# Kernel tuning notes

Measured on AMD Instinct MI355X. Metric: run time of the kernel, lower is better.

The kernel has to match this reference:

```python
import jax, jax.numpy as jnp
import numpy as np

N, H, E = 16384, 1024, 8


def setup_inputs() -> dict:
    key = jax.random.key(0)
    ks = jax.random.split(key, 6)
    scale = 0.02
    tokens = jax.random.normal(ks[0], (N, H), dtype=jnp.float32)
    gate_w = jax.random.normal(ks[1], (E, H), dtype=jnp.float32) * scale  # torch Linear weight [out,in]
    w1 = jax.random.normal(ks[2], (E, H, H), dtype=jnp.float32) * scale   # per-expert first Linear [out,in]
    b1 = jax.random.normal(ks[3], (E, H), dtype=jnp.float32) * scale
    w2 = jax.random.normal(ks[4], (E, H, H), dtype=jnp.float32) * scale   # per-expert second Linear [out,in]
    b2 = jax.random.normal(ks[5], (E, H), dtype=jnp.float32) * scale
    return {"tokens": tokens, "gate_w": gate_w, "w1": w1, "b1": b1, "w2": w2, "b2": b2}


def reference(tokens, gate_w, w1, b1, w2, b2):
    # gate: logits [N,E], top-1 routing (output is NOT scaled by gate weight, matching the torch module)
    logits = jnp.einsum('nh,eh->ne', tokens, gate_w)
    weights = jax.nn.softmax(logits, axis=-1)
    top1 = jnp.argmax(weights, axis=-1)                     # [N] int
    onehot = jax.nn.one_hot(top1, w1.shape[0], dtype=tokens.dtype)  # [N,E]
    out = jnp.zeros_like(tokens)
    for e in range(w1.shape[0]):  # small fixed expert count
        h = jax.nn.relu(jnp.einsum('nh,fh->nf', tokens, w1[e]) + b1[e])
        y = jnp.einsum('nf,gf->ng', h, w2[e]) + b2[e]
        out = out + onehot[:, e:e + 1] * y
    return out
```

## Files before the change

### kernel.cpp

```cpp
#include <hip/hip_runtime.h>
#include <hip/hip_bf16.h>
#include <stdint.h>

#define N_TOK 16384
#define HDIM  1024
#define NE    8

#define BM 128
#define BN 128
#define BK 64
#define NKT (HDIM / BK)
#define NT_N (HDIM / BN)
#define MAXTILES (N_TOK / BM + NE)
#define GRID_GEMM (MAXTILES * NT_N)

typedef __attribute__((ext_vector_type(8))) short          bf16x8;
typedef __attribute__((ext_vector_type(8))) unsigned short ushort8;
typedef __attribute__((ext_vector_type(4))) unsigned short ushort4v;
typedef __attribute__((ext_vector_type(4))) float          f32x4;

__device__ __forceinline__ unsigned short f2bf(float f) {
  union { float f; uint32_t u; } c; c.f = f;
  uint32_t u = c.u;
  uint32_t r = (u + 0x7fffu + ((u >> 16) & 1u)) >> 16;
  return (unsigned short)r;
}

__device__ __forceinline__ void gload_lds16(const void* g, void* l) {
  __builtin_amdgcn_global_load_lds((const __attribute__((address_space(1))) void*)g,
                                   (__attribute__((address_space(3))) void*)l, 16, 0, 0);
}

__device__ __forceinline__ void expert_range(const int* __restrict__ counts, int e,
                                             int& base, int& cnt) {
  int run = 0; base = 0; cnt = 0;
#pragma unroll
  for (int i = 0; i < NE; ++i) {
    int c = counts[i];
    if (i == e) { base = run; cnt = c; }
    run += c;
  }
}

__global__ __launch_bounds__(256) void gate_kernel(
    const float* __restrict__ tokens, const float* __restrict__ gate_w,
    unsigned short* __restrict__ tokB, int* __restrict__ eid)
{
  int wid  = threadIdx.x >> 6;
  int lane = threadIdx.x & 63;
  int n    = blockIdx.x * 4 + wid;

  const float* trow = tokens + (size_t)n * HDIM;
  float4 x[4];
#pragma unroll
  for (int i = 0; i < 4; ++i)
    x[i] = *(const float4*)(trow + i * 256 + lane * 4);

  unsigned short* drow = tokB + (size_t)n * HDIM;
#pragma unroll
  for (int i = 0; i < 4; ++i) {
    ushort4v o;
    o[0] = f2bf(x[i].x); o[1] = f2bf(x[i].y);
    o[2] = f2bf(x[i].z); o[3] = f2bf(x[i].w);
    *(ushort4v*)(drow + i * 256 + lane * 4) = o;
  }

  double acc[NE];
#pragma unroll
  for (int e = 0; e < NE; ++e) {
    const float* grow = gate_w + e * HDIM;
    double a = 0.0;
#pragma unroll
    for (int i = 0; i < 4; ++i) {
      float4 g = *(const float4*)(grow + i * 256 + lane * 4);
      a += (double)x[i].x * g.x + (double)x[i].y * g.y
         + (double)x[i].z * g.z + (double)x[i].w * g.w;
    }
    acc[e] = a;
  }
#pragma unroll
  for (int off = 32; off; off >>= 1) {
#pragma unroll
    for (int e = 0; e < NE; ++e) acc[e] += __shfl_xor(acc[e], off);
  }
  if (lane == 0) {
    int best = 0; double bv = acc[0];
#pragma unroll
    for (int e = 1; e < NE; ++e) if (acc[e] > bv) { bv = acc[e]; best = e; }
    eid[n] = best;
  }
}

__global__ __launch_bounds__(256) void rank_kernel(
    const int* __restrict__ eid, int* __restrict__ rank, int* __restrict__ counts)
{
  __shared__ int h[NE];
  __shared__ int bbase[NE];
  int t = threadIdx.x;
  int n = blockIdx.x * 256 + t;
  if (t < NE) h[t] = 0;
  __syncthreads();
  int e = eid[n];
  int r = atomicAdd(&h[e], 1);
  __syncthreads();
  if (t < NE) bbase[t] = atomicAdd(&counts[t], h[t]);
  __syncthreads();
  rank[n] = bbase[e] + r;
}

__global__ __launch_bounds__(256) void perm_kernel(
    const int* __restrict__ counts, const int* __restrict__ eid,
    const int* __restrict__ rank, int* __restrict__ topos)
{
  __shared__ int off[NE];
  int t = threadIdx.x;
  if (t == 0) {
    int run = 0;
#pragma unroll
    for (int e = 0; e < NE; ++e) { off[e] = run; run += counts[e]; }
  }
  __syncthreads();
  int n = blockIdx.x * 256 + t;
  topos[off[eid[n]] + rank[n]] = n;
}

__global__ void tilemap_kernel(const int* __restrict__ counts, int* __restrict__ tmeta) {
  if (threadIdx.x == 0) {
    int idx = 0;
    for (int e = 0; e < NE; ++e) {
      int ntile = (counts[e] + BM - 1) / BM;
      for (int mt = 0; mt < ntile; ++mt) tmeta[1 + idx++] = (mt << 3) | e;
    }
    tmeta[0] = idx;
  }
}

__global__ __launch_bounds__(256) void cvt2_kernel(
    const float* __restrict__ w1, const float* __restrict__ w2,
    unsigned short* __restrict__ w1B, unsigned short* __restrict__ w2B)
{
  int b = blockIdx.x;
  const float* src; unsigned short* dst; size_t i;
  if (b < 4096) { src = w1; dst = w1B; i = (size_t)b * 256 + threadIdx.x; }
  else          { src = w2; dst = w2B; i = (size_t)(b - 4096) * 256 + threadIdx.x; }
  const float4* s = (const float4*)src + i * 2;
  float4 a = s[0], c = s[1];
  ushort8 o;
  o[0] = f2bf(a.x); o[1] = f2bf(a.y); o[2] = f2bf(a.z); o[3] = f2bf(a.w);
  o[4] = f2bf(c.x); o[5] = f2bf(c.y); o[6] = f2bf(c.z); o[7] = f2bf(c.w);
  ((ushort8*)dst)[i] = o;
}

#define GEMM_PREAMBLE()                                                        \
  int bid = blockIdx.x;                                                        \
  int logical = (bid & 7) * (GRID_GEMM / 8) + (bid >> 3);                      \
  int tile = logical >> 3;                                                     \
  int nt   = logical & 7;                                                      \
  if (tile >= tmeta[0]) return;                                                \
  int ent = tmeta[1 + tile];                                                   \
  int e = ent & 7, mt = ent >> 3;                                              \
  int base, cnt;                                                               \
  expert_range(counts, e, base, cnt);                                          \
  __shared__ unsigned short Alds[BM * BK];                                     \
  __shared__ unsigned short Blds[BN * BK];                                     \
  int t    = threadIdx.x;                                                      \
  int kc   = t & 7;                                  \
  int rowi = t >> 3;                                                \
  int sch  = kc ^ (rowi & 7);               \
  int lane = t & 63, wid = t >> 6;                                             \
  int wr = wid >> 1, wc = wid & 1;                                             \
  f32x4 acc[4][4] = {};                                                        \
  int arow0 = wr * 64 + (lane & 15);                                           \
  int brow0 = wc * 64 + (lane & 15);                                           \
  int hi    = lane >> 4;                                             \
  int xo    = lane & 7;

#define GEMM_STAGE(kt)                                                         \
  _Pragma("unroll")                                                            \
  for (int r = 0; r < 4; ++r) {                                                \
    gload_lds16(APTR(r, kt), Alds + t * 8 + 2048 * r);                         \
    gload_lds16(bsrc + (size_t)(kt) * BK + (size_t)(32 * r) * HDIM,            \
                Blds + t * 8 + 2048 * r);                                      \
  }

#define GEMM_COMPUTE()                                                         \
  _Pragma("unroll")                                                            \
  for (int ks = 0; ks < 2; ++ks) {                                             \
    int ch = ((ks * 4 + hi) ^ xo) * 8;                                         \
    bf16x8 af[4], bv[4];                                                       \
    _Pragma("unroll")                                                          \
    for (int m = 0; m < 4; ++m)                                                \
      af[m] = *(const bf16x8*)(Alds + (arow0 + m * 16) * BK + ch);             \
    _Pragma("unroll")                                                          \
    for (int n2 = 0; n2 < 4; ++n2)                                             \
      bv[n2] = *(const bf16x8*)(Blds + (brow0 + n2 * 16) * BK + ch);           \
    _Pragma("unroll")                                                          \
    for (int m = 0; m < 4; ++m)                                                \
      _Pragma("unroll")                                                        \
      for (int n2 = 0; n2 < 4; ++n2)                                           \
        acc[m][n2] = __builtin_amdgcn_mfma_f32_16x16x32_bf16(                  \
            af[m], bv[n2], acc[m][n2], 0, 0, 0);                               \
  }

#define GEMM_MAINLOOP()                                                        \
  for (int kt = 0; kt < NKT; ++kt) {                                           \
    __syncthreads();                                                           \
    GEMM_STAGE(kt);                                                            \
    __syncthreads();                                                           \
    GEMM_COMPUTE();                                                            \
  }

__global__ __launch_bounds__(256) void gemm1_kernel(
    const unsigned short* __restrict__ tokB,
    const unsigned short* __restrict__ w1B,
    const float* __restrict__ b1,
    const int* __restrict__ counts,
    const int* __restrict__ tmeta,
    const int* __restrict__ topos,
    unsigned short* __restrict__ Hbuf)
{
  GEMM_PREAMBLE()
  int tokr[4];
#pragma unroll
  for (int r = 0; r < 4; ++r) {
    int pos = base + mt * BM + rowi + 32 * r;
    if (pos > N_TOK - 1) pos = N_TOK - 1;
    tokr[r] = topos[pos];
  }
  const unsigned short* bsrc =
      w1B + ((size_t)e << 20) + (size_t)(nt * BN + rowi) * HDIM + sch * 8;
#define APTR(r, kt) (tokB + (size_t)tokr[r] * HDIM + (kt) * BK + sch * 8)
  GEMM_MAINLOOP()
#undef APTR

  int crow0 = wr * 64 + (lane >> 4) * 4;
  int ccol0 = wc * 64 + (lane & 15);
  float bias[4];
#pragma unroll
  for (int n2 = 0; n2 < 4; ++n2)
    bias[n2] = b1[e * HDIM + nt * BN + ccol0 + n2 * 16];
#pragma unroll
  for (int m = 0; m < 4; ++m) {
#pragma unroll
    for (int j = 0; j < 4; ++j) {
      int row = crow0 + m * 16 + j;
      if (mt * BM + row < cnt) {
        size_t orow = (size_t)(base + mt * BM + row) * HDIM + nt * BN;
#pragma unroll
        for (int n2 = 0; n2 < 4; ++n2) {
          float v = acc[m][n2][j] + bias[n2];
          v = v > 0.f ? v : 0.f;
          Hbuf[orow + ccol0 + n2 * 16] = f2bf(v);
        }
      }
    }
  }
}

__global__ __launch_bounds__(256) void gemm2_kernel(
    const unsigned short* __restrict__ Hbuf,
    const unsigned short* __restrict__ w2B,
    const float* __restrict__ b2,
    const int* __restrict__ counts,
    const int* __restrict__ tmeta,
    const int* __restrict__ topos,
    float* __restrict__ out)
{
  GEMM_PREAMBLE()
  int arows[4];
#pragma unroll
  for (int r = 0; r < 4; ++r) {
    int pos = base + mt * BM + rowi + 32 * r;
    arows[r] = pos > N_TOK - 1 ? N_TOK - 1 : pos;
  }
  const unsigned short* bsrc =
      w2B + ((size_t)e << 20) + (size_t)(nt * BN + rowi) * HDIM + sch * 8;
#define APTR(r, kt) (Hbuf + (size_t)arows[r] * HDIM + (kt) * BK + sch * 8)
  GEMM_MAINLOOP()
#undef APTR

  int crow0 = wr * 64 + (lane >> 4) * 4;
  int ccol0 = wc * 64 + (lane & 15);
  float bias[4];
#pragma unroll
  for (int n2 = 0; n2 < 4; ++n2)
    bias[n2] = b2[e * HDIM + nt * BN + ccol0 + n2 * 16];
#pragma unroll
  for (int m = 0; m < 4; ++m) {
#pragma unroll
    for (int j = 0; j < 4; ++j) {
      int row = crow0 + m * 16 + j;
      if (mt * BM + row < cnt) {
        int tok = topos[base + mt * BM + row];
        size_t orow = (size_t)tok * HDIM + nt * BN;
#pragma unroll
        for (int n2 = 0; n2 < 4; ++n2)
          out[orow + ccol0 + n2 * 16] = acc[m][n2][j] + bias[n2];
      }
    }
  }
}

extern "C" void kernel_launch(void* const* d_in, const int* in_sizes, int n_in,
                              void* d_out, int out_size, void* d_ws, size_t ws_size,
                              hipStream_t stream) {
  (void)in_sizes; (void)n_in; (void)out_size; (void)ws_size;
  const float* tokens = (const float*)d_in[0];
  const float* gate_w = (const float*)d_in[1];
  const float* w1     = (const float*)d_in[2];
  const float* b1     = (const float*)d_in[3];
  const float* w2     = (const float*)d_in[4];
  const float* b2     = (const float*)d_in[5];
  float* out          = (float*)d_out;

  char* ws = (char*)d_ws;
  size_t o = 0;
  int* counts = (int*)(ws + o); o += 256;
  int* tmeta  = (int*)(ws + o); o += 1024;
  int* eid    = (int*)(ws + o); o += (size_t)N_TOK * 4;
  int* rank   = (int*)(ws + o); o += (size_t)N_TOK * 4;
  int* topos  = (int*)(ws + o); o += (size_t)N_TOK * 4;
  unsigned short* tokB = (unsigned short*)(ws + o); o += (size_t)N_TOK * HDIM * 2;
  unsigned short* w1B  = (unsigned short*)(ws + o); o += (size_t)NE * HDIM * HDIM * 2;
  unsigned short* w2B  = (unsigned short*)(ws + o); o += (size_t)NE * HDIM * HDIM * 2;
  unsigned short* Hbuf = (unsigned short*)(ws + o); o += (size_t)N_TOK * HDIM * 2;

  hipMemsetAsync(counts, 0, 64, stream);
  gate_kernel<<<N_TOK / 4, 256, 0, stream>>>(tokens, gate_w, tokB, eid);
  cvt2_kernel<<<8192, 256, 0, stream>>>(w1, w2, w1B, w2B);
  rank_kernel<<<N_TOK / 256, 256, 0, stream>>>(eid, rank, counts);
  perm_kernel<<<N_TOK / 256, 256, 0, stream>>>(counts, eid, rank, topos);
  tilemap_kernel<<<1, 64, 0, stream>>>(counts, tmeta);
  gemm1_kernel<<<GRID_GEMM, 256, 0, stream>>>(tokB, w1B, b1, counts, tmeta, topos, Hbuf);
  gemm2_kernel<<<GRID_GEMM, 256, 0, stream>>>(Hbuf, w2B, b2, counts, tmeta, topos, out);
}
```

Before: 178.3 us.

## Double-buffer GEMM LDS loads and pre-gather tokens into expert-contiguous buffer

The GEMM main loop now uses two LDS buffers. It prefetches two k-tiles ahead and relies on vmcnt waits, which replaces the two full syncthreads per k-step and overlaps global-to-LDS loads with MFMA work. Both GEMMs also raise wave priority around the MFMA block. The permutation kernel additionally copies bf16 token rows into a compacted, expert-sorted buffer, so gemm1 reads contiguous rows instead of gathering through topos. In exchange there is an extra 32MB copy pass and twice the LDS footprint, which may reduce occupancy.

```diff
diff --git a/kernel.cpp b/kernel.cpp
--- a/kernel.cpp
+++ b/kernel.cpp
@@ -108,20 +108,27 @@
   rank[n] = bbase[e] + r;
 }
 
-__global__ __launch_bounds__(256) void perm_kernel(
+__global__ __launch_bounds__(256) void perm_compact_kernel(
     const int* __restrict__ counts, const int* __restrict__ eid,
-    const int* __restrict__ rank, int* __restrict__ topos)
+    const int* __restrict__ rank, const unsigned short* __restrict__ tokB,
+    unsigned short* __restrict__ tokC, int* __restrict__ topos)
 {
   __shared__ int off[NE];
   int t = threadIdx.x;
-  if (t == 0) {
+  if (t < NE) {
     int run = 0;
-#pragma unroll
-    for (int e = 0; e < NE; ++e) { off[e] = run; run += counts[e]; }
+    for (int i = 0; i < t; ++i) run += counts[i];
+    off[t] = run;
   }
   __syncthreads();
-  int n = blockIdx.x * 256 + t;
-  topos[off[eid[n]] + rank[n]] = n;
+  int wid = t >> 6, lane = t & 63;
+  int n = blockIdx.x * 4 + wid;
+  int dst = off[eid[n]] + rank[n];
+  if (lane == 0) topos[dst] = n;
+  const ushort8* s = (const ushort8*)(tokB + (size_t)n * HDIM);
+  ushort8* d = (ushort8*)(tokC + (size_t)dst * HDIM);
+  d[lane]      = s[lane];
+  d[lane + 64] = s[lane + 64];
 }
 
 __global__ void tilemap_kernel(const int* __restrict__ counts, int* __restrict__ tmeta) {
@@ -161,8 +168,8 @@
   int e = ent & 7, mt = ent >> 3;                                              \
   int base, cnt;                                                               \
   expert_range(counts, e, base, cnt);                                          \
-  __shared__ unsigned short Alds[BM * BK];                                     \
-  __shared__ unsigned short Blds[BN * BK];                                     \
+  __shared__ unsigned short Alds[2][BM * BK];                                  \
+  __shared__ unsigned short Blds[2][BN * BK];                                  \
   int t    = threadIdx.x;                                                      \
   int kc   = t & 7;                                  \
   int rowi = t >> 3;                                                \
@@ -175,63 +182,70 @@
   int hi    = lane >> 4;                                             \
   int xo    = lane & 7;
 
-#define GEMM_STAGE(kt)                                                         \
+#define GEMM_STAGE(buf, kt)                                                    \
   _Pragma("unroll")                                                            \
   for (int r = 0; r < 4; ++r) {                                                \
-    gload_lds16(APTR(r, kt), Alds + t * 8 + 2048 * r);                         \
+    gload_lds16(aptr[r] + (size_t)(kt) * BK, &Alds[buf][t * 8 + 2048 * r]);    \
     gload_lds16(bsrc + (size_t)(kt) * BK + (size_t)(32 * r) * HDIM,            \
-                Blds + t * 8 + 2048 * r);                                      \
-  }
-
-#define GEMM_COMPUTE()                                                         \
+                &Blds[buf][t * 8 + 2048 * r]);                                 \
+  }
+
+#define GEMM_COMPUTE(buf)                                                      \
   _Pragma("unroll")                                                            \
   for (int ks = 0; ks < 2; ++ks) {                                             \
     int ch = ((ks * 4 + hi) ^ xo) * 8;                                         \
     bf16x8 af[4], bv[4];                                                       \
     _Pragma("unroll")                                                          \
     for (int m = 0; m < 4; ++m)                                                \
-      af[m] = *(const bf16x8*)(Alds + (arow0 + m * 16) * BK + ch);             \
+      af[m] = *(const bf16x8*)(&Alds[buf][(arow0 + m * 16) * BK + ch]);        \
     _Pragma("unroll")                                                          \
     for (int n2 = 0; n2 < 4; ++n2)                                             \
-      bv[n2] = *(const bf16x8*)(Blds + (brow0 + n2 * 16) * BK + ch);           \
+      bv[n2] = *(const bf16x8*)(&Blds[buf][(brow0 + n2 * 16) * BK + ch]);      \
+    __builtin_amdgcn_s_setprio(1);                                             \
     _Pragma("unroll")                                                          \
     for (int m = 0; m < 4; ++m)                                                \
       _Pragma("unroll")                                                        \
       for (int n2 = 0; n2 < 4; ++n2)                                           \
         acc[m][n2] = __builtin_amdgcn_mfma_f32_16x16x32_bf16(                  \
             af[m], bv[n2], acc[m][n2], 0, 0, 0);                               \
+    __builtin_amdgcn_s_setprio(0);                                             \
   }
 
 #define GEMM_MAINLOOP()                                                        \
+  GEMM_STAGE(0, 0);                                                            \
+  GEMM_STAGE(1, 1);                                                            \
   for (int kt = 0; kt < NKT; ++kt) {                                           \
-    __syncthreads();                                                           \
-    GEMM_STAGE(kt);                                                            \
-    __syncthreads();                                                           \
-    GEMM_COMPUTE();                                                            \
+    if (kt == NKT - 1) asm volatile("s_waitcnt vmcnt(0)" ::: "memory");        \
+    else               asm volatile("s_waitcnt vmcnt(8)" ::: "memory");        \
+    __builtin_amdgcn_s_barrier();                                              \
+    __builtin_amdgcn_sched_barrier(0);                                         \
+    GEMM_COMPUTE(kt & 1);                                                      \
+    if (kt < NKT - 2) {                                                        \
+      __builtin_amdgcn_s_barrier();                                            \
+      __builtin_amdgcn_sched_barrier(0);                                       \
+      GEMM_STAGE(kt & 1, kt + 2);                                              \
+    }                                                                          \
   }
 
 __global__ __launch_bounds__(256) void gemm1_kernel(
-    const unsigned short* __restrict__ tokB,
+    const unsigned short* __restrict__ tokC,
     const unsigned short* __restrict__ w1B,
     const float* __restrict__ b1,
     const int* __restrict__ counts,
     const int* __restrict__ tmeta,
-    const int* __restrict__ topos,
     unsigned short* __restrict__ Hbuf)
 {
   GEMM_PREAMBLE()
-  int tokr[4];
+  const unsigned short* aptr[4];
 #pragma unroll
   for (int r = 0; r < 4; ++r) {
     int pos = base + mt * BM + rowi + 32 * r;
     if (pos > N_TOK - 1) pos = N_TOK - 1;
-    tokr[r] = topos[pos];
+    aptr[r] = tokC + (size_t)pos * HDIM + sch * 8;
   }
   const unsigned short* bsrc =
       w1B + ((size_t)e << 20) + (size_t)(nt * BN + rowi) * HDIM + sch * 8;
-#define APTR(r, kt) (tokB + (size_t)tokr[r] * HDIM + (kt) * BK + sch * 8)
   GEMM_MAINLOOP()
-#undef APTR
 
   int crow0 = wr * 64 + (lane >> 4) * 4;
   int ccol0 = wc * 64 + (lane & 15);
@@ -267,17 +281,16 @@
     float* __restrict__ out)
 {
   GEMM_PREAMBLE()
-  int arows[4];
+  const unsigned short* aptr[4];
 #pragma unroll
   for (int r = 0; r < 4; ++r) {
     int pos = base + mt * BM + rowi + 32 * r;
-    arows[r] = pos > N_TOK - 1 ? N_TOK - 1 : pos;
+    if (pos > N_TOK - 1) pos = N_TOK - 1;
+    aptr[r] = Hbuf + (size_t)pos * HDIM + sch * 8;
   }
   const unsigned short* bsrc =
       w2B + ((size_t)e << 20) + (size_t)(nt * BN + rowi) * HDIM + sch * 8;
-#define APTR(r, kt) (Hbuf + (size_t)arows[r] * HDIM + (kt) * BK + sch * 8)
   GEMM_MAINLOOP()
-#undef APTR
 
   int crow0 = wr * 64 + (lane >> 4) * 4;
   int ccol0 = wc * 64 + (lane & 15);
@@ -321,6 +334,7 @@
   int* rank   = (int*)(ws + o); o += (size_t)N_TOK * 4;
   int* topos  = (int*)(ws + o); o += (size_t)N_TOK * 4;
   unsigned short* tokB = (unsigned short*)(ws + o); o += (size_t)N_TOK * HDIM * 2;
+  unsigned short* tokC = (unsigned short*)(ws + o); o += (size_t)N_TOK * HDIM * 2;
   unsigned short* w1B  = (unsigned short*)(ws + o); o += (size_t)NE * HDIM * HDIM * 2;
   unsigned short* w2B  = (unsigned short*)(ws + o); o += (size_t)NE * HDIM * HDIM * 2;
   unsigned short* Hbuf = (unsigned short*)(ws + o); o += (size_t)N_TOK * HDIM * 2;
@@ -329,8 +343,8 @@
   gate_kernel<<<N_TOK / 4, 256, 0, stream>>>(tokens, gate_w, tokB, eid);
   cvt2_kernel<<<8192, 256, 0, stream>>>(w1, w2, w1B, w2B);
   rank_kernel<<<N_TOK / 256, 256, 0, stream>>>(eid, rank, counts);
-  perm_kernel<<<N_TOK / 256, 256, 0, stream>>>(counts, eid, rank, topos);
+  perm_compact_kernel<<<N_TOK / 4, 256, 0, stream>>>(counts, eid, rank, tokB, tokC, topos);
   tilemap_kernel<<<1, 64, 0, stream>>>(counts, tmeta);
-  gemm1_kernel<<<GRID_GEMM, 256, 0, stream>>>(tokB, w1B, b1, counts, tmeta, topos, Hbuf);
+  gemm1_kernel<<<GRID_GEMM, 256, 0, stream>>>(tokC, w1B, b1, counts, tmeta, Hbuf);
   gemm2_kernel<<<GRID_GEMM, 256, 0, stream>>>(Hbuf, w2B, b2, counts, tmeta, topos, out);
 }
```

Result: slower. 204.5 us (+14.7%).
